# Kernel tuning notes

Measured on AMD Instinct MI355X. Metric: run time of the kernel, lower is better.

## Reference

```python
import jax, jax.numpy as jnp
import numpy as np

LMBDA = 0.25  # from init_kwargs


def setup_inputs() -> dict:
    key = jax.random.key(0)
    k1, k2 = jax.random.split(key)
    N, K, D = 131072, 512, 256
    embeddings = jax.random.normal(k1, (N, D), dtype=jnp.float32)
    centroids = jax.random.normal(k2, (K, D), dtype=jnp.float32)
    return {"embeddings": embeddings, "centroids": centroids}


def reference(embeddings, centroids):
    # distances[n,k] = lmbda * sum_d (e[n,d] - c[k,d])^2
    # expanded form avoids materializing the [N,K,D] broadcast intermediate:
    # |e-c|^2 = |e|^2 + |c|^2 - 2 e.c
    e_sq = jnp.sum(embeddings * embeddings, axis=1)  # [N]
    c_sq = jnp.sum(centroids * centroids, axis=1)    # [K]
    cross = jnp.einsum('nd,kd->nk', embeddings, centroids)  # [N,K]
    distances = LMBDA * (e_sq[:, None] + c_sq[None, :] - 2.0 * cross)  # [N,K]
    cluster_distances = jnp.max(distances, axis=1)          # [N]
    cluster_assignments = jnp.argmax(distances, axis=1)     # [N], int
    loss = LMBDA * jnp.sum(cluster_distances)  # note: lmbda applied twice, as in source
    return loss, jax.lax.stop_gradient(cluster_assignments)
```

## Files before the change

kernel.cpp:

```cpp
#include <hip/hip_runtime.h>

#define ND 256
#define NK 512
#define LM2 0.0625f
#define DELTA 0.25f

typedef _Float16 f16x8 __attribute__((ext_vector_type(8)));
typedef float f32x4 __attribute__((ext_vector_type(4)));
typedef unsigned short u16x8 __attribute__((ext_vector_type(8)));
typedef unsigned short u16x4 __attribute__((ext_vector_type(4)));

#define GLD16(GSRC, LDST)                                                      \
    __builtin_amdgcn_global_load_lds(                                         \
        (const __attribute__((address_space(1))) void*)(GSRC),                \
        (__attribute__((address_space(3))) void*)(LDST), 16, 0, 0)

__global__ __launch_bounds__(64) void prep_kernel(const float* __restrict__ Cg,
                                                  float* __restrict__ csq,
                                                  unsigned short* __restrict__ Cf) {
    const int k = blockIdx.x, lane = threadIdx.x;
    float4 v = *(const float4*)(Cg + (size_t)k * ND + lane * 4);
    float s = v.x * v.x + v.y * v.y + v.z * v.z + v.w * v.w;
#pragma unroll
    for (int m = 1; m <= 32; m <<= 1) s += __shfl_xor(s, m, 64);
    if (lane == 0) csq[k] = s;
    u16x4 h;
    h[0] = __builtin_bit_cast(unsigned short, (_Float16)v.x);
    h[1] = __builtin_bit_cast(unsigned short, (_Float16)v.y);
    h[2] = __builtin_bit_cast(unsigned short, (_Float16)v.z);
    h[3] = __builtin_bit_cast(unsigned short, (_Float16)v.w);
    const int panel = k >> 6, col = k & 63;
    const int krow = (lane >> 3) * 4 + ((lane >> 1) & 3);
    const size_t idx = ((size_t)panel << 14) + ((((size_t)krow << 6) + col) << 3) + ((lane & 1) << 2);
    *(u16x4*)(Cf + idx) = h;
}

__global__ __launch_bounds__(256, 2) void kmeans_mfma(
    const float* __restrict__ E, const unsigned short* __restrict__ Cf,
    const float* __restrict__ csq, uint2* __restrict__ partials,
    float* __restrict__ e2s) {
    __shared__ unsigned short Bbuf[2][16384];

    const int tid = threadIdx.x;
    const int lane = tid & 63, wid = tid >> 6;
    const int l15 = lane & 15, l4 = lane >> 4;
    const int rowbase = blockIdx.x << 7;
    const int wrow = rowbase + wid * 32;

    {
        const unsigned short* gsrc = Cf;
#pragma unroll
        for (int i = 0; i < 8; ++i)
            GLD16(gsrc + (((size_t)(wid * 8 + i) * 64 + lane) << 3),
                  &Bbuf[0][(size_t)(wid * 8 + i) << 9]);
    }

    const float* a0 = E + (size_t)(wrow + l15) * ND + l4 * 8;
    const float* a1 = E + (size_t)(wrow + 16 + l15) * ND + l4 * 8;

    f16x8 A[2][8];
    float e2 = 0.f;
#pragma unroll
    for (int m = 0; m < 2; ++m) {
        const float* ap = m ? a1 : a0;
#pragma unroll
        for (int half = 0; half < 2; ++half) {
            float4 t[8];
#pragma unroll
            for (int q = 0; q < 4; ++q) {
                t[q * 2]     = *(const float4*)(ap + (half * 4 + q) * 32);
                t[q * 2 + 1] = *(const float4*)(ap + (half * 4 + q) * 32 + 4);
            }
#pragma unroll
            for (int q = 0; q < 4; ++q) {
                float4 v0 = t[q * 2], v1 = t[q * 2 + 1];
                e2 += v0.x * v0.x + v0.y * v0.y + v0.z * v0.z + v0.w * v0.w +
                      v1.x * v1.x + v1.y * v1.y + v1.z * v1.z + v1.w * v1.w;
                u16x8 h;
                h[0] = __builtin_bit_cast(unsigned short, (_Float16)v0.x);
                h[1] = __builtin_bit_cast(unsigned short, (_Float16)v0.y);
                h[2] = __builtin_bit_cast(unsigned short, (_Float16)v0.z);
                h[3] = __builtin_bit_cast(unsigned short, (_Float16)v0.w);
                h[4] = __builtin_bit_cast(unsigned short, (_Float16)v1.x);
                h[5] = __builtin_bit_cast(unsigned short, (_Float16)v1.y);
                h[6] = __builtin_bit_cast(unsigned short, (_Float16)v1.z);
                h[7] = __builtin_bit_cast(unsigned short, (_Float16)v1.w);
                A[m][half * 4 + q] = __builtin_bit_cast(f16x8, h);
            }
        }
    }

    unsigned k1[2][4], k2[2][4];
#pragma unroll
    for (int m = 0; m < 2; ++m)
#pragma unroll
        for (int j = 0; j < 4; ++j) { k1[m][j] = 0u; k2[m][j] = 0u; }

#pragma unroll 1
    for (int p = 0; p < 8; ++p) {
        __syncthreads();
        if (p < 7) {
            const unsigned short* gsrc = Cf + ((size_t)(p + 1) << 14);
            unsigned short* ldst = (unsigned short*)Bbuf[(p + 1) & 1];
#pragma unroll
            for (int i = 0; i < 8; ++i)
                GLD16(gsrc + (((size_t)(wid * 8 + i) * 64 + lane) << 3),
                      &ldst[(size_t)(wid * 8 + i) << 9]);
        }
        float csp[4];
        unsigned ck[4];
#pragma unroll
        for (int n = 0; n < 4; ++n) {
            const int col = (p << 6) + n * 16 + l15;
            csp[n] = csq[col];
            ck[n] = (unsigned)(NK - 1 - col);
        }
        const unsigned short* cur = Bbuf[p & 1];
        f32x4 acc[2][4] = {};
#pragma unroll
        for (int ks = 0; ks < 8; ++ks) {
            u16x8 bf[4];
#pragma unroll
            for (int n = 0; n < 4; ++n)
                bf[n] = *(const u16x8*)&cur[(size_t)((((ks << 2) + l4) << 6) + n * 16 + l15) << 3];
#pragma unroll
            for (int m = 0; m < 2; ++m)
#pragma unroll
                for (int n = 0; n < 4; ++n)
                    acc[m][n] = __builtin_amdgcn_mfma_f32_16x16x32_f16(
                        A[m][ks], __builtin_bit_cast(f16x8, bf[n]), acc[m][n], 0, 0, 0);
        }
#pragma unroll
        for (int m = 0; m < 2; ++m)
#pragma unroll
            for (int j = 0; j < 4; ++j)
#pragma unroll
                for (int n = 0; n < 4; ++n) {
                    const float s = fmaf(-2.f, acc[m][n][j], csp[n]);
                    const unsigned b = __builtin_bit_cast(unsigned, s);
                    const unsigned mono = b ^ ((unsigned)((int)b >> 31) | 0x80000000u);
                    const unsigned key = (mono & 0xFFFFFE00u) | ck[n];
                    const unsigned mn = min(k1[m][j], key);
                    k1[m][j] = max(k1[m][j], key);
                    k2[m][j] = max(k2[m][j], mn);
                }
    }

#pragma unroll
    for (int m = 0; m < 2; ++m)
#pragma unroll
        for (int j = 0; j < 4; ++j) {
            unsigned a = k1[m][j], b2 = k2[m][j];
#pragma unroll
            for (int mk = 1; mk <= 8; mk <<= 1) {
                const unsigned oa = __shfl_xor(a, mk, 64);
                const unsigned ob = __shfl_xor(b2, mk, 64);
                const unsigned mn = min(a, oa);
                a = max(a, oa);
                b2 = max(max(b2, ob), mn);
            }
            if (l15 == 0) {
                const int row = wrow + m * 16 + l4 * 4 + j;
                uint2 o;
                o.x = a;
                o.y = b2;
                partials[row] = o;
            }
        }

#pragma unroll
    for (int mk = 1; mk <= 32; mk <<= 1) e2 += __shfl_xor(e2, mk, 64);
    if (lane == 0) e2s[blockIdx.x * 4 + wid] = e2;
}

__global__ __launch_bounds__(256) void combine_kernel(
    const uint2* __restrict__ partials, const float* __restrict__ csq,
    const float* __restrict__ E, const float* __restrict__ Cg,
    float* __restrict__ out, float* __restrict__ sum2) {
    const int n = blockIdx.x * 256 + threadIdx.x;
    const uint2 kk = partials[n];
    const unsigned m1 = kk.x & 0xFFFFFE00u;
    float v1 = __builtin_bit_cast(float, (m1 & 0x80000000u) ? (m1 ^ 0x80000000u) : ~m1);
    int i1 = (int)(NK - 1) - (int)(kk.x & 511u);
    const unsigned m2 = kk.y & 0xFFFFFE00u;
    const float v2 = __builtin_bit_cast(float, (m2 & 0x80000000u) ? (m2 ^ 0x80000000u) : ~m2);
    const int i2 = (int)(NK - 1) - (int)(kk.y & 511u);

    if (v1 - v2 <= DELTA) {
        const float* e = E + (size_t)n * ND;
        const float* c1p = Cg + (size_t)i1 * ND;
        const float* c2p = Cg + (size_t)i2 * ND;
        float d1 = 0.f, d2 = 0.f;
        for (int d = 0; d < ND; d += 4) {
            float4 ev = *(const float4*)(e + d);
            float4 cv1 = *(const float4*)(c1p + d);
            float4 cv2 = *(const float4*)(c2p + d);
            d1 += ev.x * cv1.x + ev.y * cv1.y + ev.z * cv1.z + ev.w * cv1.w;
            d2 += ev.x * cv2.x + ev.y * cv2.y + ev.z * cv2.z + ev.w * cv2.w;
        }
        const float s1 = csq[i1] - 2.f * d1;
        const float s2 = csq[i2] - 2.f * d2;
        if (s2 > s1 || (s2 == s1 && i2 < i1)) { v1 = s2; i1 = i2; } else { v1 = s1; }
    }
    out[1 + n] = (float)i1;
    float s = v1;
#pragma unroll
    for (int mk = 1; mk <= 32; mk <<= 1) s += __shfl_xor(s, mk, 64);
    __shared__ float wsm[4];
    const int lane = threadIdx.x & 63, wd = threadIdx.x >> 6;
    if (lane == 0) wsm[wd] = s;
    __syncthreads();
    if (threadIdx.x == 0) sum2[blockIdx.x] = wsm[0] + wsm[1] + wsm[2] + wsm[3];
}

__global__ __launch_bounds__(256) void final_kernel(const float* __restrict__ e2s,
                                                    const float* __restrict__ sum2,
                                                    float* __restrict__ out) {
    float s = 0.f;
    for (int i = threadIdx.x; i < 4096; i += 256) s += e2s[i];
    for (int i = threadIdx.x; i < 512; i += 256) s += sum2[i];
#pragma unroll
    for (int mk = 1; mk <= 32; mk <<= 1) s += __shfl_xor(s, mk, 64);
    __shared__ float wsm[4];
    const int lane = threadIdx.x & 63, wd = threadIdx.x >> 6;
    if (lane == 0) wsm[wd] = s;
    __syncthreads();
    if (threadIdx.x == 0) out[0] = LM2 * (wsm[0] + wsm[1] + wsm[2] + wsm[3]);
}

extern "C" void kernel_launch(void* const* d_in, const int* in_sizes, int n_in,
                              void* d_out, int out_size, void* d_ws, size_t ws_size,
                              hipStream_t stream) {
    (void)n_in; (void)out_size; (void)ws_size;
    const float* E = (const float*)d_in[0];
    const float* Cg = (const float*)d_in[1];
    float* out = (float*)d_out;

    float* wsf = (float*)d_ws;
    float* csq = wsf;
    float* e2s = wsf + 512;
    float* sum2 = wsf + 4608;
    unsigned short* Cf = (unsigned short*)(wsf + 5120);
    uint2* partials = (uint2*)(wsf + 5120 + 65536);

    const int N = in_sizes[0] / ND;
    const int nblk = N >> 7;

    prep_kernel<<<NK, 64, 0, stream>>>(Cg, csq, Cf);
    kmeans_mfma<<<nblk, 256, 0, stream>>>(E, Cf, csq, partials, e2s);
    combine_kernel<<<N / 256, 256, 0, stream>>>(partials, csq, E, Cg, out, sum2);
    final_kernel<<<1, 256, 0, stream>>>(e2s, sum2, out);
}
```

Baseline: 104.8 us.

## Split MFMA work to 16 rows per wave with 8-wave blocks

```diff
diff --git a/kernel.cpp b/kernel.cpp
--- a/kernel.cpp
+++ b/kernel.cpp
@@ -35,7 +35,7 @@
     *(u16x4*)(Cf + idx) = h;
 }
 
-__global__ __launch_bounds__(256, 2) void kmeans_mfma(
+__global__ __launch_bounds__(512, 4) void kmeans_mfma(
     const float* __restrict__ E, const unsigned short* __restrict__ Cf,
     const float* __restrict__ csq, uint2* __restrict__ partials,
     float* __restrict__ e2s) {
@@ -45,56 +45,46 @@
     const int lane = tid & 63, wid = tid >> 6;
     const int l15 = lane & 15, l4 = lane >> 4;
     const int rowbase = blockIdx.x << 7;
-    const int wrow = rowbase + wid * 32;
-
-    {
-        const unsigned short* gsrc = Cf;
-#pragma unroll
-        for (int i = 0; i < 8; ++i)
-            GLD16(gsrc + (((size_t)(wid * 8 + i) * 64 + lane) << 3),
-                  &Bbuf[0][(size_t)(wid * 8 + i) << 9]);
-    }
-
-    const float* a0 = E + (size_t)(wrow + l15) * ND + l4 * 8;
-    const float* a1 = E + (size_t)(wrow + 16 + l15) * ND + l4 * 8;
-
-    f16x8 A[2][8];
+    const int wrow = rowbase + wid * 16;
+
+#pragma unroll
+    for (int i = 0; i < 4; ++i)
+        GLD16(Cf + (((size_t)(wid * 4 + i) * 64 + lane) << 3),
+              &Bbuf[0][(size_t)(wid * 4 + i) << 9]);
+
+    const float* ap = E + (size_t)(wrow + l15) * ND + l4 * 8;
+
+    f16x8 A[8];
     float e2 = 0.f;
 #pragma unroll
-    for (int m = 0; m < 2; ++m) {
-        const float* ap = m ? a1 : a0;
-#pragma unroll
-        for (int half = 0; half < 2; ++half) {
-            float4 t[8];
-#pragma unroll
-            for (int q = 0; q < 4; ++q) {
-                t[q * 2]     = *(const float4*)(ap + (half * 4 + q) * 32);
-                t[q * 2 + 1] = *(const float4*)(ap + (half * 4 + q) * 32 + 4);
-            }
-#pragma unroll
-            for (int q = 0; q < 4; ++q) {
-                float4 v0 = t[q * 2], v1 = t[q * 2 + 1];
-                e2 += v0.x * v0.x + v0.y * v0.y + v0.z * v0.z + v0.w * v0.w +
-                      v1.x * v1.x + v1.y * v1.y + v1.z * v1.z + v1.w * v1.w;
-                u16x8 h;
-                h[0] = __builtin_bit_cast(unsigned short, (_Float16)v0.x);
-                h[1] = __builtin_bit_cast(unsigned short, (_Float16)v0.y);
-                h[2] = __builtin_bit_cast(unsigned short, (_Float16)v0.z);
-                h[3] = __builtin_bit_cast(unsigned short, (_Float16)v0.w);
-                h[4] = __builtin_bit_cast(unsigned short, (_Float16)v1.x);
-                h[5] = __builtin_bit_cast(unsigned short, (_Float16)v1.y);
-                h[6] = __builtin_bit_cast(unsigned short, (_Float16)v1.z);
-                h[7] = __builtin_bit_cast(unsigned short, (_Float16)v1.w);
-                A[m][half * 4 + q] = __builtin_bit_cast(f16x8, h);
-            }
-        }
-    }
-
-    unsigned k1[2][4], k2[2][4];
-#pragma unroll
-    for (int m = 0; m < 2; ++m)
-#pragma unroll
-        for (int j = 0; j < 4; ++j) { k1[m][j] = 0u; k2[m][j] = 0u; }
+    for (int half = 0; half < 2; ++half) {
+        float4 t[8];
+#pragma unroll
+        for (int q = 0; q < 4; ++q) {
+            t[q * 2]     = *(const float4*)(ap + (half * 4 + q) * 32);
+            t[q * 2 + 1] = *(const float4*)(ap + (half * 4 + q) * 32 + 4);
+        }
+#pragma unroll
+        for (int q = 0; q < 4; ++q) {
+            float4 v0 = t[q * 2], v1 = t[q * 2 + 1];
+            e2 += v0.x * v0.x + v0.y * v0.y + v0.z * v0.z + v0.w * v0.w +
+                  v1.x * v1.x + v1.y * v1.y + v1.z * v1.z + v1.w * v1.w;
+            u16x8 h;
+            h[0] = __builtin_bit_cast(unsigned short, (_Float16)v0.x);
+            h[1] = __builtin_bit_cast(unsigned short, (_Float16)v0.y);
+            h[2] = __builtin_bit_cast(unsigned short, (_Float16)v0.z);
+            h[3] = __builtin_bit_cast(unsigned short, (_Float16)v0.w);
+            h[4] = __builtin_bit_cast(unsigned short, (_Float16)v1.x);
+            h[5] = __builtin_bit_cast(unsigned short, (_Float16)v1.y);
+            h[6] = __builtin_bit_cast(unsigned short, (_Float16)v1.z);
+            h[7] = __builtin_bit_cast(unsigned short, (_Float16)v1.w);
+            A[half * 4 + q] = __builtin_bit_cast(f16x8, h);
+        }
+    }
+
+    unsigned k1[4], k2[4];
+#pragma unroll
+    for (int j = 0; j < 4; ++j) { k1[j] = 0u; k2[j] = 0u; }
 
 #pragma unroll 1
     for (int p = 0; p < 8; ++p) {
@@ -103,9 +93,9 @@
             const unsigned short* gsrc = Cf + ((size_t)(p + 1) << 14);
             unsigned short* ldst = (unsigned short*)Bbuf[(p + 1) & 1];
 #pragma unroll
-            for (int i = 0; i < 8; ++i)
-                GLD16(gsrc + (((size_t)(wid * 8 + i) * 64 + lane) << 3),
-                      &ldst[(size_t)(wid * 8 + i) << 9]);
+            for (int i = 0; i < 4; ++i)
+                GLD16(gsrc + (((size_t)(wid * 4 + i) * 64 + lane) << 3),
+                      &ldst[(size_t)(wid * 4 + i) << 9]);
         }
         float csp[4];
         unsigned ck[4];
@@ -116,7 +106,7 @@
             ck[n] = (unsigned)(NK - 1 - col);
         }
         const unsigned short* cur = Bbuf[p & 1];
-        f32x4 acc[2][4] = {};
+        f32x4 acc[4] = {};
 #pragma unroll
         for (int ks = 0; ks < 8; ++ks) {
             u16x8 bf[4];
@@ -124,53 +114,47 @@
             for (int n = 0; n < 4; ++n)
                 bf[n] = *(const u16x8*)&cur[(size_t)((((ks << 2) + l4) << 6) + n * 16 + l15) << 3];
 #pragma unroll
-            for (int m = 0; m < 2; ++m)
-#pragma unroll
-                for (int n = 0; n < 4; ++n)
-                    acc[m][n] = __builtin_amdgcn_mfma_f32_16x16x32_f16(
-                        A[m][ks], __builtin_bit_cast(f16x8, bf[n]), acc[m][n], 0, 0, 0);
-        }
-#pragma unroll
-        for (int m = 0; m < 2; ++m)
-#pragma unroll
-            for (int j = 0; j < 4; ++j)
-#pragma unroll
-                for (int n = 0; n < 4; ++n) {
-                    const float s = fmaf(-2.f, acc[m][n][j], csp[n]);
-                    const unsigned b = __builtin_bit_cast(unsigned, s);
-                    const unsigned mono = b ^ ((unsigned)((int)b >> 31) | 0x80000000u);
-                    const unsigned key = (mono & 0xFFFFFE00u) | ck[n];
-                    const unsigned mn = min(k1[m][j], key);
-                    k1[m][j] = max(k1[m][j], key);
-                    k2[m][j] = max(k2[m][j], mn);
-                }
-    }
-
-#pragma unroll
-    for (int m = 0; m < 2; ++m)
-#pragma unroll
-        for (int j = 0; j < 4; ++j) {
-            unsigned a = k1[m][j], b2 = k2[m][j];
-#pragma unroll
-            for (int mk = 1; mk <= 8; mk <<= 1) {
-                const unsigned oa = __shfl_xor(a, mk, 64);
-                const unsigned ob = __shfl_xor(b2, mk, 64);
-                const unsigned mn = min(a, oa);
-                a = max(a, oa);
-                b2 = max(max(b2, ob), mn);
+            for (int n = 0; n < 4; ++n)
+                acc[n] = __builtin_amdgcn_mfma_f32_16x16x32_f16(
+                    A[ks], __builtin_bit_cast(f16x8, bf[n]), acc[n], 0, 0, 0);
+        }
+#pragma unroll
+        for (int j = 0; j < 4; ++j)
+#pragma unroll
+            for (int n = 0; n < 4; ++n) {
+                const float s = fmaf(-2.f, acc[n][j], csp[n]);
+                const unsigned b = __builtin_bit_cast(unsigned, s);
+                const unsigned mono = b ^ ((unsigned)((int)b >> 31) | 0x80000000u);
+                const unsigned key = (mono & 0xFFFFFE00u) | ck[n];
+                const unsigned mn = min(k1[j], key);
+                k1[j] = max(k1[j], key);
+                k2[j] = max(k2[j], mn);
             }
-            if (l15 == 0) {
-                const int row = wrow + m * 16 + l4 * 4 + j;
-                uint2 o;
-                o.x = a;
-                o.y = b2;
-                partials[row] = o;
-            }
-        }
+    }
+
+#pragma unroll
+    for (int j = 0; j < 4; ++j) {
+        unsigned a = k1[j], b2 = k2[j];
+#pragma unroll
+        for (int mk = 1; mk <= 8; mk <<= 1) {
+            const unsigned oa = __shfl_xor(a, mk, 64);
+            const unsigned ob = __shfl_xor(b2, mk, 64);
+            const unsigned mn = min(a, oa);
+            a = max(a, oa);
+            b2 = max(max(b2, ob), mn);
+        }
+        if (l15 == 0) {
+            const int row = wrow + l4 * 4 + j;
+            uint2 o;
+            o.x = a;
+            o.y = b2;
+            partials[row] = o;
+        }
+    }
 
 #pragma unroll
     for (int mk = 1; mk <= 32; mk <<= 1) e2 += __shfl_xor(e2, mk, 64);
-    if (lane == 0) e2s[blockIdx.x * 4 + wid] = e2;
+    if (lane == 0) e2s[blockIdx.x * 8 + wid] = e2;
 }
 
 __global__ __launch_bounds__(256) void combine_kernel(
@@ -217,7 +201,7 @@
                                                     const float* __restrict__ sum2,
                                                     float* __restrict__ out) {
     float s = 0.f;
-    for (int i = threadIdx.x; i < 4096; i += 256) s += e2s[i];
+    for (int i = threadIdx.x; i < 8192; i += 256) s += e2s[i];
     for (int i = threadIdx.x; i < 512; i += 256) s += sum2[i];
 #pragma unroll
     for (int mk = 1; mk <= 32; mk <<= 1) s += __shfl_xor(s, mk, 64);
@@ -239,15 +223,15 @@
     float* wsf = (float*)d_ws;
     float* csq = wsf;
     float* e2s = wsf + 512;
-    float* sum2 = wsf + 4608;
-    unsigned short* Cf = (unsigned short*)(wsf + 5120);
-    uint2* partials = (uint2*)(wsf + 5120 + 65536);
+    float* sum2 = wsf + 8704;
+    unsigned short* Cf = (unsigned short*)(wsf + 9216);
+    uint2* partials = (uint2*)(wsf + 9216 + 65536);
 
     const int N = in_sizes[0] / ND;
     const int nblk = N >> 7;
 
     prep_kernel<<<NK, 64, 0, stream>>>(Cg, csq, Cf);
-    kmeans_mfma<<<nblk, 256, 0, stream>>>(E, Cf, csq, partials, e2s);
+    kmeans_mfma<<<nblk, 512, 0, stream>>>(E, Cf, csq, partials, e2s);
     combine_kernel<<<N / 256, 256, 0, stream>>>(partials, csq, E, Cg, out, sum2);
     final_kernel<<<1, 256, 0, stream>>>(e2s, sum2, out);
 }
```

Result: faster. 100.2 us (-4.4%).
